# Performance work log

Hardware: AMD Instinct MI355X
Metric: run time of the kernel (lower is better)

The kernel has to match this reference:

```python
import jax, jax.numpy as jnp
import numpy as np

N = 20000       # nodes
E = 262144      # edges
DA, DV, DD = 128, 64, 32
R = 16          # CP rank of TensorProds
NRAD = 8        # radial basis size (hardcoded 8 in module)
R0 = 5.0        # cutoff radius r0


def setup_inputs() -> dict:
    key = jax.random.key(0)
    ks = jax.random.split(key, 13)
    nrm = lambda k, shape, fan: jax.random.normal(k, shape, jnp.float32) / np.sqrt(fan)
    return {
        'r_ij': jax.random.normal(ks[0], (E, 3), jnp.float32),
        'x_a': jax.random.normal(ks[1], (N, DA), jnp.float32),
        'x_v': jax.random.normal(ks[2], (N, DV, 3), jnp.float32),
        'x_d': jax.random.normal(ks[3], (N, DD, 3, 3), jnp.float32),
        'W1_a': nrm(ks[4], (3, R, DA), DA),   # tp_000, tp_011, tp_022 (rank-0 input)
        'W1_v': nrm(ks[5], (4, R, DV), DV),   # tp_101, tp_110, tp_112, tp_121
        'W1_d': nrm(ks[6], (4, R, DD), DD),   # tp_202, tp_211, tp_220, tp_222
        'W2': nrm(ks[7], (11, R, NRAD), NRAD),  # radial-side proj for all 11 TPs
        'Wo_a': nrm(ks[8], (3, DA, R), R),    # outputs of tp_000, tp_110, tp_220
        'Wo_v': nrm(ks[9], (4, DV, R), R),    # outputs of tp_011, tp_101, tp_121, tp_211
        'Wo_d': nrm(ks[10], (4, DD, R), R),   # outputs of tp_022, tp_112, tp_202, tp_222
        'src': jax.random.randint(ks[11], (E,), 0, N),
        'dst': jax.random.randint(ks[12], (E,), 0, N),
    }


def tens_sigmoid_vec(v, eps=1e-6):
    # direction-preserving bounded nonlinearity on rank-1 tensors
    n = jnp.linalg.norm(v, axis=-1, keepdims=True)
    return v * (2.0 * jax.nn.sigmoid(n) - 1.0) / (n + eps)


def _forward(r_ij, x_a, x_v, x_d, W1_a, W1_v, W1_d, W2, Wo_a, Wo_v, Wo_d, src, dst):
    n_nodes = x_a.shape[0]
    # radial_encode_edge(r, 8, r0)
    npi = jnp.pi * jnp.arange(NRAD, dtype=jnp.float32)
    x_sq = jnp.sum(r_ij * r_ij, -1) / R0                       # (E,)
    rad = jnp.cos(npi * jnp.sqrt(x_sq)[:, None]) * jax.nn.relu(1.0 - x_sq)[:, None]  # (E,8)
    rv = tens_sigmoid_vec(r_ij * (17.0 / R0))                  # (E,3)
    phi_a = rad                                                # (E,8)
    phi_v = rad[..., None] * rv[:, None, :]                    # (E,8,3)
    phi_d = rad[..., None, None] * rv[:, None, None, :] * rv[:, None, :, None]  # (E,8,3,3)
    # edges_read_dst: gather node features at destination nodes
    xa_j, xv_j, xd_j = x_a[dst], x_v[dst], x_d[dst]
    p1 = lambda W, x: jnp.einsum('rc,ec...->er...', W, x)      # channel->CP-rank proj
    outp = lambda Wo, t: jnp.einsum('dr,er...->ed...', Wo, t)  # CP-rank->channel proj
    p2a = lambda i: jnp.einsum('rc,ec->er', W2[i], phi_a)
    p2v = lambda i: jnp.einsum('rc,eci->eri', W2[i], phi_v)
    p2d = lambda i: jnp.einsum('rc,ecij->erij', W2[i], phi_d)
    # W2 index order: 000,110,220,011,101,121,211,022,112,202,222
    pa000, pa011, pa022 = p1(W1_a[0], xa_j), p1(W1_a[1], xa_j), p1(W1_a[2], xa_j)
    pv101, pv110, pv112, pv121 = (p1(W1_v[i], xv_j) for i in range(4))
    pd202, pd211, pd220, pd222 = (p1(W1_d[i], xd_j) for i in range(4))
    psi_a = (outp(Wo_a[0], pa000 * p2a(0))
             + outp(Wo_a[1], jnp.einsum('eri,eri->er', pv110, p2v(1)))
             + outp(Wo_a[2], jnp.einsum('erij,erij->er', pd220, p2d(2))))
    psi_v = (outp(Wo_v[0], pa011[..., None] * p2v(3))
             + outp(Wo_v[1], pv101 * p2a(4)[..., None])
             + outp(Wo_v[2], jnp.einsum('eri,erij->erj', pv121, p2d(5)))
             + outp(Wo_v[3], jnp.einsum('erij,erj->eri', pd211, p2v(6))))
    psi_d = (outp(Wo_d[0], pa022[..., None, None] * p2d(7))
             + outp(Wo_d[1], jnp.einsum('eri,erj->erij', pv112, p2v(8)))
             + outp(Wo_d[2], pd202 * p2a(9)[..., None, None])
             + outp(Wo_d[3], jnp.einsum('erik,erkj->erij', pd222, p2d(10))))
    # edges_reduce_src: scatter-add messages to source nodes
    B_a = jax.ops.segment_sum(psi_a, src, num_segments=n_nodes)
    B_v = jax.ops.segment_sum(psi_v, src, num_segments=n_nodes)
    B_d = jax.ops.segment_sum(psi_d, src, num_segments=n_nodes)
    return (B_a, B_v, B_d)


def reference(r_ij, x_a, x_v, x_d, W1_a, W1_v, W1_d, W2, Wo_a, Wo_v, Wo_d, src, dst):
    return _forward(r_ij, x_a, x_v, x_d, W1_a, W1_v, W1_d, W2, Wo_a, Wo_v, Wo_d, src, dst)
```

## Files before the change

### kernel.cpp

```cpp
#include <hip/hip_runtime.h>
#include <hip/hip_bf16.h>
#include <math.h>

#define PI_F 3.14159265358979323846f
#define R0_F 5.0f


static __device__ __forceinline__ float dot4(float4 a, float4 b) {
  return a.x * b.x + a.y * b.y + a.z * b.z + a.w * b.w;
}

__global__ __launch_bounds__(256) void node_proj_kernel(
    const float* __restrict__ x_a, const float* __restrict__ x_v, const float* __restrict__ x_d,
    const float* __restrict__ W1_a, const float* __restrict__ W1_v, const float* __restrict__ W1_d,
    float* __restrict__ P, int N)
{
  __shared__ float S[12352];
  const int tid = threadIdx.x;
  const int lane = tid & 63;
  const int wu = __builtin_amdgcn_readfirstlane(tid >> 6);
  const int n0 = blockIdx.x * 64;
  const int nrem = min(N - n0, 64);

  for (int idx4 = tid; idx4 < nrem * 32; idx4 += 256) {
    int n = idx4 >> 5, c4 = idx4 & 31;
    float4 v = ((const float4*)(x_a + (size_t)(n0 + n) * 128))[c4];
    float* d = &S[n * 129 + c4 * 4];
    d[0] = v.x; d[1] = v.y; d[2] = v.z; d[3] = v.w;
  }
  __syncthreads();
  {
    float acc[12];
    #pragma unroll
    for (int q = 0; q < 12; q++) acc[q] = 0.0f;
    const float* xrow = &S[lane * 129];
    for (int c0 = 0; c0 < 128; c0 += 16) {
      float xr[16];
      #pragma unroll
      for (int j = 0; j < 16; j++) xr[j] = xrow[c0 + j];
      #pragma unroll
      for (int q = 0; q < 12; q++) {
        int o = wu * 12 + q;
        const float* wp = W1_a + (o >> 4) * 2048 + (o & 15) * 128 + c0;
        float s = 0.0f;
        #pragma unroll
        for (int j = 0; j < 16; j++) s += wp[j] * xr[j];
        acc[q] += s;
      }
    }
    __syncthreads();
    #pragma unroll
    for (int q = 0; q < 12; q++) S[lane * 49 + wu * 12 + q] = acc[q];
    __syncthreads();
    for (int u = tid; u < nrem * 12; u += 256) {
      int n = u / 12, m4 = u - n * 12;
      const float* s = &S[n * 49 + m4 * 4];
      ((float4*)(P + (size_t)(n0 + n) * 816))[m4] = make_float4(s[0], s[1], s[2], s[3]);
    }
  }
  __syncthreads();

  for (int idx4 = tid; idx4 < nrem * 48; idx4 += 256) {
    int n = idx4 / 48, m4 = idx4 - n * 48;
    float4 v = ((const float4*)(x_v + (size_t)(n0 + n) * 192))[m4];
    float* d = &S[n * 193 + m4 * 4];
    d[0] = v.x; d[1] = v.y; d[2] = v.z; d[3] = v.w;
  }
  __syncthreads();
  {
    float acc[16][3];
    #pragma unroll
    for (int r = 0; r < 16; r++)
      #pragma unroll
      for (int i = 0; i < 3; i++) acc[r][i] = 0.0f;
    const float* xrow = &S[lane * 193];
    for (int c0 = 0; c0 < 64; c0 += 16) {
      float xr[16][3];
      #pragma unroll
      for (int j = 0; j < 16; j++) {
        xr[j][0] = xrow[(c0 + j) * 3 + 0];
        xr[j][1] = xrow[(c0 + j) * 3 + 1];
        xr[j][2] = xrow[(c0 + j) * 3 + 2];
      }
      #pragma unroll
      for (int r = 0; r < 16; r++) {
        const float* wp = W1_v + wu * 1024 + r * 64 + c0;
        #pragma unroll
        for (int j = 0; j < 16; j++) {
          float w = wp[j];
          acc[r][0] += w * xr[j][0];
          acc[r][1] += w * xr[j][1];
          acc[r][2] += w * xr[j][2];
        }
      }
    }
    __syncthreads();
    #pragma unroll
    for (int r = 0; r < 16; r++)
      #pragma unroll
      for (int i = 0; i < 3; i++)
        S[lane * 193 + wu * 48 + r * 3 + i] = acc[r][i];
    __syncthreads();
    for (int u = tid; u < nrem * 48; u += 256) {
      int n = u / 48, m4 = u - n * 48;
      const float* s = &S[n * 193 + m4 * 4];
      ((float4*)(P + (size_t)(n0 + n) * 816 + 48))[m4] = make_float4(s[0], s[1], s[2], s[3]);
    }
  }
  __syncthreads();

  for (int idx = tid; idx < nrem * 160; idx += 256) {
    int n = idx / 160, m = idx - n * 160, c = m / 5, ij = m - c * 5;
    S[n * 161 + m] = x_d[(size_t)(n0 + n) * 288 + c * 9 + ij];
  }
  __syncthreads();
  {
    float acc[16][5];
    #pragma unroll
    for (int r = 0; r < 16; r++)
      #pragma unroll
      for (int t = 0; t < 5; t++) acc[r][t] = 0.0f;
    const float* xrow = &S[lane * 161];
    for (int c0 = 0; c0 < 32; c0 += 8) {
      float xr[8][5];
      #pragma unroll
      for (int j = 0; j < 8; j++)
        #pragma unroll
        for (int t = 0; t < 5; t++) xr[j][t] = xrow[(c0 + j) * 5 + t];
      #pragma unroll
      for (int r = 0; r < 16; r++) {
        const float* wp = W1_d + wu * 512 + r * 32 + c0;
        #pragma unroll
        for (int j = 0; j < 8; j++) {
          float w = wp[j];
          #pragma unroll
          for (int t = 0; t < 5; t++) acc[r][t] += w * xr[j][t];
        }
      }
    }
    #pragma unroll
    for (int h = 0; h < 2; h++) {
      __syncthreads();
      if ((lane >> 5) == h) {
        int l5 = lane & 31;
        #pragma unroll
        for (int r = 0; r < 16; r++)
          #pragma unroll
          for (int t = 0; t < 5; t++)
            S[l5 * 321 + wu * 80 + r * 5 + t] = acc[r][t];
      }
      __syncthreads();
      int nbase = h * 32;
      int cnt = min(nrem - nbase, 32);
      for (int u = tid; u < cnt * 320; u += 256) {
        int n = u / 320, m = u - n * 320;
        int kk = m / 80, mm = m - kk * 80, rr = mm / 5, t = mm - rr * 5;
        P[(size_t)(n0 + nbase + n) * 816 + 240 + kk * 144 + 9 * rr + t] = S[n * 321 + m];
      }
    }
  }
  __syncthreads();

  for (int idx = tid; idx < nrem * 128; idx += 256) {
    int n = idx >> 7, m = idx & 127, c = m >> 2, t = m & 3;
    S[n * 129 + m] = x_d[(size_t)(n0 + n) * 288 + c * 9 + 5 + t];
  }
  __syncthreads();
  {
    float acc[16][4];
    #pragma unroll
    for (int r = 0; r < 16; r++)
      #pragma unroll
      for (int t = 0; t < 4; t++) acc[r][t] = 0.0f;
    const float* xrow = &S[lane * 129];
    for (int c0 = 0; c0 < 32; c0 += 8) {
      float xr[8][4];
      #pragma unroll
      for (int j = 0; j < 8; j++)
        #pragma unroll
        for (int t = 0; t < 4; t++) xr[j][t] = xrow[(c0 + j) * 4 + t];
      #pragma unroll
      for (int r = 0; r < 16; r++) {
        const float* wp = W1_d + wu * 512 + r * 32 + c0;
        #pragma unroll
        for (int j = 0; j < 8; j++) {
          float w = wp[j];
          #pragma unroll
          for (int t = 0; t < 4; t++) acc[r][t] += w * xr[j][t];
        }
      }
    }
    #pragma unroll
    for (int h = 0; h < 2; h++) {
      __syncthreads();
      if ((lane >> 5) == h) {
        int l5 = lane & 31;
        #pragma unroll
        for (int r = 0; r < 16; r++)
          #pragma unroll
          for (int t = 0; t < 4; t++)
            S[l5 * 257 + wu * 64 + r * 4 + t] = acc[r][t];
      }
      __syncthreads();
      int nbase = h * 32;
      int cnt = min(nrem - nbase, 32);
      for (int u = tid; u < cnt * 256; u += 256) {
        int n = u >> 8, m = u & 255;
        int kk = m >> 6, mm = m & 63, rr = mm >> 2, t = mm & 3;
        P[(size_t)(n0 + nbase + n) * 816 + 240 + kk * 144 + 9 * rr + 5 + t] = S[n * 257 + m];
      }
    }
  }
}

__global__ void hist_kernel(const int* __restrict__ src, int* __restrict__ counts, int E) {
  int e = blockIdx.x * 256 + threadIdx.x;
  if (e < E) atomicAdd(&counts[src[e]], 1);
}

__global__ __launch_bounds__(1024) void scan_kernel(
    const int* __restrict__ counts, int* __restrict__ offs, int* __restrict__ cursor,
    int N, int E)
{
  __shared__ int part[1024];
  int tid = threadIdx.x;
  int chunk = (N + 1023) / 1024;
  int lo = tid * chunk, hi = min(lo + chunk, N);
  int s = 0;
  for (int i = lo; i < hi; i++) s += counts[i];
  part[tid] = s;
  __syncthreads();
  for (int off = 1; off < 1024; off <<= 1) {
    int v = (tid >= off) ? part[tid - off] : 0;
    __syncthreads();
    part[tid] += v;
    __syncthreads();
  }
  int run = part[tid] - s;
  for (int i = lo; i < hi; i++) { offs[i] = run; cursor[i] = run; run += counts[i]; }
  if (tid == 0) offs[N] = E;
}

__global__ void scatter_kernel(const int* __restrict__ src, int* __restrict__ cursor,
                               int* __restrict__ eidx, int E) {
  int e = blockIdx.x * 256 + threadIdx.x;
  if (e < E) { int p = atomicAdd(&cursor[src[e]], 1); eidx[p] = e; }
}

__global__ __launch_bounds__(64, 3) void node_gather_kernel(
    const float* __restrict__ r_ij, const int* __restrict__ dst,
    const int* __restrict__ offs, const int* __restrict__ eidx,
    const float* __restrict__ Pg, const float* __restrict__ W2,
    const float* __restrict__ Wo_a, const float* __restrict__ Wo_v, const float* __restrict__ Wo_d,
    float* __restrict__ out, int N)
{
  __shared__ __align__(16) float S[1280];
  float4* S4 = (float4*)S;
  const int n = blockIdx.x, lane = threadIdx.x;
  const int off = offs[n], deg = offs[n + 1] - off;

  int aP[12], aQ[12], aF[12];
  unsigned typm = 0;
  #pragma unroll
  for (int p = 0; p < 3; p++) {
    int t = lane + 64 * p;
    int k = t / 48, m = t - 48 * k, jj = m >> 4, r = m & 15;
    int q_ = 816 + (3 + k) * 16 + r;
    int P_, F_;
    if (k == 0)      { P_ = 16 + r;              F_ = 992 + jj; }
    else if (k == 1) { P_ = 48 + 3 * r + jj;     F_ = 995; }
    else if (k == 2) { P_ = 192 + 3 * r;         F_ = 992 + jj; typm |= 1u << p; }
    else             { P_ = 384 + 9 * r + 3 * jj; F_ = 995;     typm |= 1u << p; }
    aP[p] = P_; aQ[p] = q_; aF[p] = F_;
  }
  #pragma unroll
  for (int p = 0; p < 9; p++) {
    int u = lane + 64 * p;
    int s = u / 144, m = u - 144 * s, ij = m >> 4, r = m & 15;
    int i = ij / 3, jj = ij - 3 * i;
    int P_, F_, q_;
    if (s == 0)      { P_ = 32 + r;              q_ = 112 + r; F_ = 996 + ij; }
    else if (s == 1) { P_ = 144 + 3 * r + i;     q_ = 128 + r; F_ = 992 + jj; }
    else if (s == 2) { P_ = 240 + 9 * r + ij;    q_ = 144 + r; F_ = 995; }
    else             { P_ = 672 + 9 * r + 3 * i; q_ = 160 + r; F_ = 992 + jj; typm |= 1u << (3 + p); }
    aP[3 + p] = P_; aQ[3 + p] = 816 + q_; aF[3 + p] = F_;
  }
  const int ak = lane >> 4, ar = lane & 15;

  float4 wqa[3], wqb[3];
  #pragma unroll
  for (int p = 0; p < 3; p++) {
    int tq = lane + 64 * p; if (tq > 175) tq = 175;
    const float4* w = (const float4*)(W2 + tq * 8);
    wqa[p] = w[0]; wqb[p] = w[1];
  }

  float accA = 0.0f, acc[12];
  #pragma unroll
  for (int p = 0; p < 12; p++) acc[p] = 0.0f;

  float4 pb0 = {}, pb1 = {}, pb2 = {}, pb3 = {};
  const int l3 = 192 + (lane < 12 ? lane : 0);

  for (int base = 0; base < deg; base += 64) {
    int cnt = min(deg - base, 64);
    __syncthreads();
    if (lane < cnt) {
      int e = eidx[off + base + lane];
      float a = r_ij[3 * (size_t)e], b = r_ij[3 * (size_t)e + 1], c = r_ij[3 * (size_t)e + 2];
      S4[252 + lane] = make_float4(a, b, c, __int_as_float(dst[e]));
    }
    __syncthreads();
    {
      float4 me = S4[252];
      if (me.x * me.x + me.y * me.y + me.z * me.z < 5.0f) {
        const float4* Pp = (const float4*)(Pg + (size_t)__float_as_int(me.w) * 816);
        pb0 = Pp[lane]; pb1 = Pp[64 + lane]; pb2 = Pp[128 + lane]; pb3 = Pp[l3];
      }
    }
    for (int t = 0; t < cnt; t++) {
      float4 me = S4[252 + t];
      float r0 = me.x, r1 = me.y, r2 = me.z;
      float rr = r0 * r0 + r1 * r1 + r2 * r2;
      bool live = rr < 5.0f;
      float rv0 = 0, rv1 = 0, rv2 = 0;
      if (live) {
        float x_sq = rr * (1.0f / R0_F);
        float env = 1.0f - x_sq;
        float v0 = r0 * (17.0f / R0_F), v1 = r1 * (17.0f / R0_F), v2 = r2 * (17.0f / R0_F);
        float nn = sqrtf(v0 * v0 + v1 * v1 + v2 * v2);
        float sig = 2.0f / (1.0f + __expf(-nn)) - 1.0f;
        float sc = sig / (nn + 1e-6f);
        rv0 = v0 * sc; rv1 = v1 * sc; rv2 = v2 * sc;
        float rad[8];
        {
          float c1 = __cosf(PI_F * sqrtf(x_sq));
          float two_c1 = 2.0f * c1, cm2 = 1.0f, cm1 = c1;
          rad[0] = env; rad[1] = c1 * env;
          #pragma unroll
          for (int k = 2; k < 8; k++) { float c = two_c1 * cm1 - cm2; rad[k] = c * env; cm2 = cm1; cm1 = c; }
        }
        float4 ra = make_float4(rad[0], rad[1], rad[2], rad[3]);
        float4 rb = make_float4(rad[4], rad[5], rad[6], rad[7]);
        S4[lane] = pb0; S4[64 + lane] = pb1; S4[128 + lane] = pb2;
        if (lane < 12) S4[192 + lane] = pb3;
        S[816 + lane] = dot4(wqa[0], ra) + dot4(wqb[0], rb);
        S[880 + lane] = dot4(wqa[1], ra) + dot4(wqb[1], rb);
        if (lane < 48) S[944 + lane] = dot4(wqa[2], ra) + dot4(wqb[2], rb);
        if (lane < 4) S[992 + lane] = (lane == 0) ? rv0 : (lane == 1) ? rv1 : (lane == 2) ? rv2 : 1.0f;
        if (lane >= 4 && lane < 13) {
          int ij = lane - 4, i = ij / 3, j = ij - 3 * i;
          float a = (i == 0) ? rv0 : (i == 1) ? rv1 : rv2;
          float b = (j == 0) ? rv0 : (j == 1) ? rv1 : rv2;
          S[992 + lane] = a * b;
        }
      }
      if (t + 1 < cnt) {
        float4 m2 = S4[252 + t + 1];
        if (m2.x * m2.x + m2.y * m2.y + m2.z * m2.z < 5.0f) {
          const float4* Pp = (const float4*)(Pg + (size_t)__float_as_int(m2.w) * 816);
          pb0 = Pp[lane]; pb1 = Pp[64 + lane]; pb2 = Pp[128 + lane]; pb3 = Pp[l3];
        }
      }
      __syncthreads();
      if (live) {
        if (lane < 48) {
          float v;
          if (ak == 0)      v = S[ar] * S[816 + ar];
          else if (ak == 1) v = (S[96 + 3 * ar] * rv0 + S[97 + 3 * ar] * rv1 + S[98 + 3 * ar] * rv2) * S[832 + ar];
          else {
            int b = 528 + 9 * ar;
            float o = (S[b] * rv0 + S[b + 3] * rv1 + S[b + 6] * rv2) * rv0
                    + (S[b + 1] * rv0 + S[b + 4] * rv1 + S[b + 7] * rv2) * rv1
                    + (S[b + 2] * rv0 + S[b + 5] * rv1 + S[b + 8] * rv2) * rv2;
            v = o * S[848 + ar];
          }
          accA += v;
        }
        #pragma unroll
        for (int p = 0; p < 12; p++) {
          float pv;
          if (typm & (1u << p)) pv = S[aP[p]] * rv0 + S[aP[p] + 1] * rv1 + S[aP[p] + 2] * rv2;
          else                  pv = S[aP[p]];
          acc[p] += pv * S[aQ[p]] * S[aF[p]];
        }
      }
      __syncthreads();
    }
  }

  __syncthreads();
  if (lane < 48) S[lane] = accA;
  #pragma unroll
  for (int p = 0; p < 3; p++) S[48 + lane + 64 * p] = acc[p];
  #pragma unroll
  for (int p = 0; p < 9; p++) {
    int u = lane + 64 * p;
    int s = u / 144, m = u - 144 * s, ij = m >> 4, r = m & 15;
    S[240 + s * 180 + ij * 20 + r] = acc[3 + p];
  }
  __syncthreads();

  const size_t baseV = (size_t)N * 128;
  const size_t baseD = (size_t)N * 320;

  #pragma unroll
  for (int h = 0; h < 2; h++) {
    int c = lane + 64 * h;
    float a_ = 0.0f;
    #pragma unroll
    for (int k = 0; k < 3; k++) {
      const float4* w = (const float4*)(Wo_a + k * 2048 + c * 16);
      const float4* A4 = (const float4*)(&S[k * 16]);
      #pragma unroll
      for (int cc = 0; cc < 4; cc++) a_ += dot4(w[cc], A4[cc]);
    }
    out[(size_t)n * 128 + c] = a_;
  }
  {
    float o0 = 0, o1 = 0, o2 = 0;
    #pragma unroll
    for (int k = 0; k < 4; k++) {
      const float4* w = (const float4*)(Wo_v + k * 1024 + lane * 16);
      float4 w0 = w[0], w1 = w[1], w2 = w[2], w3 = w[3];
      #pragma unroll
      for (int j = 0; j < 3; j++) {
        const float4* A4 = (const float4*)(&S[48 + k * 48 + j * 16]);
        float v = dot4(w0, A4[0]) + dot4(w1, A4[1]) + dot4(w2, A4[2]) + dot4(w3, A4[3]);
        if (j == 0) o0 += v; else if (j == 1) o1 += v; else o2 += v;
      }
    }
    size_t ov = baseV + (size_t)n * 192 + lane * 3;
    out[ov] = o0; out[ov + 1] = o1; out[ov + 2] = o2;
  }
  #pragma unroll
  for (int p = 0; p < 5; p++) {
    int t = lane + 64 * p;
    if (t < 288) {
      int d = t / 9, ij = t - 9 * d;
      float a_ = 0.0f;
      #pragma unroll
      for (int s = 0; s < 4; s++) {
        const float4* w = (const float4*)(Wo_d + s * 512 + d * 16);
        const float4* A4 = (const float4*)(&S[240 + s * 180 + ij * 20]);
        a_ += dot4(w[0], A4[0]) + dot4(w[1], A4[1]) + dot4(w[2], A4[2]) + dot4(w[3], A4[3]);
      }
      out[baseD + (size_t)n * 288 + t] = a_;
    }
  }
}

extern "C" void kernel_launch(void* const* d_in, const int* in_sizes, int n_in,
                              void* d_out, int out_size, void* d_ws, size_t ws_size,
                              hipStream_t stream) {
  const float* r_ij = (const float*)d_in[0];
  const float* x_a  = (const float*)d_in[1];
  const float* x_v  = (const float*)d_in[2];
  const float* x_d  = (const float*)d_in[3];
  const float* W1_a = (const float*)d_in[4];
  const float* W1_v = (const float*)d_in[5];
  const float* W1_d = (const float*)d_in[6];
  const float* W2   = (const float*)d_in[7];
  const float* Wo_a = (const float*)d_in[8];
  const float* Wo_v = (const float*)d_in[9];
  const float* Wo_d = (const float*)d_in[10];
  const int*  src   = (const int*)d_in[11];
  const int*  dst   = (const int*)d_in[12];

  const int E = in_sizes[0] / 3;
  const int N = in_sizes[1] / 128;

  float* P    = (float*)d_ws;
  int* counts = (int*)(P + (size_t)N * 816);
  int* offs   = counts + N;
  int* cursor = offs + N + 1;
  int* eidx   = cursor + N;

  hipMemsetAsync(counts, 0, sizeof(int) * (size_t)N, stream);

  hist_kernel<<<(E + 255) / 256, 256, 0, stream>>>(src, counts, E);
  scan_kernel<<<1, 1024, 0, stream>>>(counts, offs, cursor, N, E);
  scatter_kernel<<<(E + 255) / 256, 256, 0, stream>>>(src, cursor, eidx, E);
  node_proj_kernel<<<(N + 63) / 64, 256, 0, stream>>>(x_a, x_v, x_d, W1_a, W1_v, W1_d, P, N);
  node_gather_kernel<<<N, 64, 0, stream>>>(r_ij, dst, offs, eidx, P, W2,
                                           Wo_a, Wo_v, Wo_d, (float*)d_out, N);
}
```

Measured before the change: 475.4 us.

## Pack four nodes per 256-thread block in gather kernel

The gather kernel now runs four nodes per block, one wavefront each, instead of one 64-thread block per node. Each wave has its own shared-memory slice. Because block-wide __syncthreads remain, all waves loop to the maximum degree among the four nodes, with inactive iterations masked off. The aim is to cut per-block launch overhead and raise occupancy, at the cost of load imbalance when degrees differ and of barriers coupling the waves together.

```diff
diff --git a/kernel.cpp b/kernel.cpp
--- a/kernel.cpp
+++ b/kernel.cpp
@@ -247,17 +247,24 @@
   if (e < E) { int p = atomicAdd(&cursor[src[e]], 1); eidx[p] = e; }
 }
 
-__global__ __launch_bounds__(64, 3) void node_gather_kernel(
+__global__ __launch_bounds__(256, 5) void node_gather_kernel(
     const float* __restrict__ r_ij, const int* __restrict__ dst,
     const int* __restrict__ offs, const int* __restrict__ eidx,
     const float* __restrict__ Pg, const float* __restrict__ W2,
     const float* __restrict__ Wo_a, const float* __restrict__ Wo_v, const float* __restrict__ Wo_d,
     float* __restrict__ out, int N)
 {
-  __shared__ __align__(16) float S[1280];
+  __shared__ __align__(16) float Sall[5120];
+  __shared__ int degs[4];
+  const int wid = threadIdx.x >> 6;
+  const int lane = threadIdx.x & 63;
+  const int n = blockIdx.x * 4 + wid;
+  const bool valid = (n < N);
+  float* S = Sall + wid * 1280;
   float4* S4 = (float4*)S;
-  const int n = blockIdx.x, lane = threadIdx.x;
-  const int off = offs[n], deg = offs[n + 1] - off;
+  const int off = valid ? offs[n] : 0;
+  const int deg = valid ? (offs[n + 1] - off) : 0;
+  if (lane == 0) degs[wid] = deg;
 
   int aP[12], aQ[12], aF[12];
   unsigned typm = 0;
@@ -302,8 +309,12 @@
   float4 pb0 = {}, pb1 = {}, pb2 = {}, pb3 = {};
   const int l3 = 192 + (lane < 12 ? lane : 0);
 
-  for (int base = 0; base < deg; base += 64) {
-    int cnt = min(deg - base, 64);
+  __syncthreads();
+  const int degmax = max(max(degs[0], degs[1]), max(degs[2], degs[3]));
+
+  for (int base = 0; base < degmax; base += 64) {
+    const int cnt = min(max(deg - base, 0), 64);
+    const int cntmax = min(degmax - base, 64);
     __syncthreads();
     if (lane < cnt) {
       int e = eidx[off + base + lane];
@@ -311,18 +322,18 @@
       S4[252 + lane] = make_float4(a, b, c, __int_as_float(dst[e]));
     }
     __syncthreads();
-    {
+    if (cnt > 0) {
       float4 me = S4[252];
       if (me.x * me.x + me.y * me.y + me.z * me.z < 5.0f) {
         const float4* Pp = (const float4*)(Pg + (size_t)__float_as_int(me.w) * 816);
         pb0 = Pp[lane]; pb1 = Pp[64 + lane]; pb2 = Pp[128 + lane]; pb3 = Pp[l3];
       }
     }
-    for (int t = 0; t < cnt; t++) {
+    for (int t = 0; t < cntmax; t++) {
       float4 me = S4[252 + t];
       float r0 = me.x, r1 = me.y, r2 = me.z;
       float rr = r0 * r0 + r1 * r1 + r2 * r2;
-      bool live = rr < 5.0f;
+      bool live = (t < cnt) && (rr < 5.0f);
       float rv0 = 0, rv1 = 0, rv2 = 0;
       if (live) {
         float x_sq = rr * (1.0f / R0_F);
@@ -401,51 +412,53 @@
   }
   __syncthreads();
 
-  const size_t baseV = (size_t)N * 128;
-  const size_t baseD = (size_t)N * 320;
-
-  #pragma unroll
-  for (int h = 0; h < 2; h++) {
-    int c = lane + 64 * h;
-    float a_ = 0.0f;
-    #pragma unroll
-    for (int k = 0; k < 3; k++) {
-      const float4* w = (const float4*)(Wo_a + k * 2048 + c * 16);
-      const float4* A4 = (const float4*)(&S[k * 16]);
-      #pragma unroll
-      for (int cc = 0; cc < 4; cc++) a_ += dot4(w[cc], A4[cc]);
-    }
-    out[(size_t)n * 128 + c] = a_;
-  }
-  {
-    float o0 = 0, o1 = 0, o2 = 0;
-    #pragma unroll
-    for (int k = 0; k < 4; k++) {
-      const float4* w = (const float4*)(Wo_v + k * 1024 + lane * 16);
-      float4 w0 = w[0], w1 = w[1], w2 = w[2], w3 = w[3];
-      #pragma unroll
-      for (int j = 0; j < 3; j++) {
-        const float4* A4 = (const float4*)(&S[48 + k * 48 + j * 16]);
-        float v = dot4(w0, A4[0]) + dot4(w1, A4[1]) + dot4(w2, A4[2]) + dot4(w3, A4[3]);
-        if (j == 0) o0 += v; else if (j == 1) o1 += v; else o2 += v;
-      }
-    }
-    size_t ov = baseV + (size_t)n * 192 + lane * 3;
-    out[ov] = o0; out[ov + 1] = o1; out[ov + 2] = o2;
-  }
-  #pragma unroll
-  for (int p = 0; p < 5; p++) {
-    int t = lane + 64 * p;
-    if (t < 288) {
-      int d = t / 9, ij = t - 9 * d;
+  if (valid) {
+    const size_t baseV = (size_t)N * 128;
+    const size_t baseD = (size_t)N * 320;
+
+    #pragma unroll
+    for (int h = 0; h < 2; h++) {
+      int c = lane + 64 * h;
       float a_ = 0.0f;
       #pragma unroll
-      for (int s = 0; s < 4; s++) {
-        const float4* w = (const float4*)(Wo_d + s * 512 + d * 16);
-        const float4* A4 = (const float4*)(&S[240 + s * 180 + ij * 20]);
-        a_ += dot4(w[0], A4[0]) + dot4(w[1], A4[1]) + dot4(w[2], A4[2]) + dot4(w[3], A4[3]);
-      }
-      out[baseD + (size_t)n * 288 + t] = a_;
+      for (int k = 0; k < 3; k++) {
+        const float4* w = (const float4*)(Wo_a + k * 2048 + c * 16);
+        const float4* A4 = (const float4*)(&S[k * 16]);
+        #pragma unroll
+        for (int cc = 0; cc < 4; cc++) a_ += dot4(w[cc], A4[cc]);
+      }
+      out[(size_t)n * 128 + c] = a_;
+    }
+    {
+      float o0 = 0, o1 = 0, o2 = 0;
+      #pragma unroll
+      for (int k = 0; k < 4; k++) {
+        const float4* w = (const float4*)(Wo_v + k * 1024 + lane * 16);
+        float4 w0 = w[0], w1 = w[1], w2 = w[2], w3 = w[3];
+        #pragma unroll
+        for (int j = 0; j < 3; j++) {
+          const float4* A4 = (const float4*)(&S[48 + k * 48 + j * 16]);
+          float v = dot4(w0, A4[0]) + dot4(w1, A4[1]) + dot4(w2, A4[2]) + dot4(w3, A4[3]);
+          if (j == 0) o0 += v; else if (j == 1) o1 += v; else o2 += v;
+        }
+      }
+      size_t ov = baseV + (size_t)n * 192 + lane * 3;
+      out[ov] = o0; out[ov + 1] = o1; out[ov + 2] = o2;
+    }
+    #pragma unroll
+    for (int p = 0; p < 5; p++) {
+      int t = lane + 64 * p;
+      if (t < 288) {
+        int d = t / 9, ij = t - 9 * d;
+        float a_ = 0.0f;
+        #pragma unroll
+        for (int s = 0; s < 4; s++) {
+          const float4* w = (const float4*)(Wo_d + s * 512 + d * 16);
+          const float4* A4 = (const float4*)(&S[240 + s * 180 + ij * 20]);
+          a_ += dot4(w[0], A4[0]) + dot4(w[1], A4[1]) + dot4(w[2], A4[2]) + dot4(w[3], A4[3]);
+        }
+        out[baseD + (size_t)n * 288 + t] = a_;
+      }
     }
   }
 }
@@ -482,6 +495,6 @@
   scan_kernel<<<1, 1024, 0, stream>>>(counts, offs, cursor, N, E);
   scatter_kernel<<<(E + 255) / 256, 256, 0, stream>>>(src, cursor, eidx, E);
   node_proj_kernel<<<(N + 63) / 64, 256, 0, stream>>>(x_a, x_v, x_d, W1_a, W1_v, W1_d, P, N);
-  node_gather_kernel<<<N, 64, 0, stream>>>(r_ij, dst, offs, eidx, P, W2,
-                                           Wo_a, Wo_v, Wo_d, (float*)d_out, N);
-}
+  node_gather_kernel<<<(N + 3) / 4, 256, 0, stream>>>(r_ij, dst, offs, eidx, P, W2,
+                                                      Wo_a, Wo_v, Wo_d, (float*)d_out, N);
+}
```

Measured after the change: 1.054 ms. +121.8%, slower.
